# Kernel optimization log

Measured on AMD Instinct MI355X. Metric: run time of the kernel, lower is better.

The kernel has to match this reference:

```python
import jax, jax.numpy as jnp
import numpy as np

HID = 16  # comparator hidden channels, Conv1(2,16) -> Conv1(16,1)


def setup_inputs() -> dict:
    key = jax.random.key(0)
    k0, k1, k2 = jax.random.split(key, 3)
    B, N = 32, 512
    x = jax.random.normal(k0, (B, 1, N), dtype=jnp.float32)
    # xavier_uniform for 1x1 convs, zero bias (as in PermNet.__init__)
    g1 = (6.0 / (2 + HID)) ** 0.5
    g2 = (6.0 / (HID + 1)) ** 0.5
    w1 = jax.random.uniform(k1, (HID, 2), jnp.float32, -g1, g1)
    b1 = jnp.zeros((HID,), jnp.float32)
    w2 = jax.random.uniform(k2, (1, HID), jnp.float32, -g2, g2)
    b2 = jnp.zeros((1,), jnp.float32)
    lr = jnp.ones((1,), jnp.float32)  # learned step size, used via abs()
    return {"x": x, "w1": w1, "b1": b1, "w2": w2, "b2": b2, "lr": lr,
            "steps": 8, "temp": 1}


def reference(x, w1, b1, w2, b2, lr, steps, temp):
    B, C, N = x.shape  # C == 1 (scalar set elements)
    temp = jnp.asarray(temp, x.dtype)

    # --- Comparator: pairwise 1x1-conv MLP over all (i, j) pairs ---
    xi = jnp.broadcast_to(x[:, 0, :, None], (B, N, N))  # element i
    xj = jnp.broadcast_to(x[:, 0, None, :], (B, N, N))  # element j
    pairs = jnp.stack([xi, xj], axis=1)                  # (B, 2, N, N)
    h = jax.nn.relu(jnp.einsum('oc,bcij->boij', w1, pairs)
                    + b1[None, :, None, None])           # (B, HID, N, N)
    c = (jnp.einsum('oc,bcij->boij', w2, h)
         + b2[None, :, None, None])[:, 0]                # (B, N, N)
    c = c - jnp.swapaxes(c, -1, -2)  # antisymmetric ordering cost C(i,j)=-C(j,i)

    # --- calculate_assignment: iterative differentiable permutation ---
    # a[b, i, k] = weight of element i being placed at position k
    lr_abs = jnp.abs(lr)[0]
    a0 = jnp.full((B, N, N), 1.0 / N, dtype=x.dtype)

    def step(a, _):
        csum = jnp.cumsum(a, axis=-1)      # sum_{l<=k} a[., j, l]
        total = csum[..., -1:]
        left = csum - a                     # sum_{l<k}
        right = total - csum                # sum_{l>k}
        m = right - left                    # (B, N, N)
        # d(total cost)/d a_{ik} = sum_j C_{ij} * (right_{jk} - left_{jk})
        grad = jnp.einsum('bij,bjk->bik', c, m)
        a_new = jax.nn.softmax((a - lr_abs * grad) / temp, axis=-1)
        return a_new, None

    a, _ = jax.lax.scan(step, a0, None, length=steps)

    # --- apply_assignment: permute elements into positions ---
    y = jnp.einsum('bci,bik->bck', x, a)  # (B, 1, N)
    return y, a
```

## Files before the change

kernel.cpp:

```cpp
#include <hip/hip_runtime.h>
#include <hip/hip_bf16.h>
#include <math.h>

#define B_   32
#define N_   512
#define HID_ 16

typedef __attribute__((ext_vector_type(8))) short bf16x8;
typedef __attribute__((ext_vector_type(4))) float f32x4;

union U8 { ushort u[8]; uint4 v; };
union U4 { ushort u[4]; uint2 v; };

__device__ __forceinline__ ushort f2bf(float f) {
    __hip_bfloat16 h = __float2bfloat16(f);
    return *reinterpret_cast<ushort*>(&h);
}
__device__ __forceinline__ float bf2f(ushort u) {
    return __uint_as_float(((unsigned int)u) << 16);
}

__device__ __forceinline__ void gload16(const void* g, void* l) {
    __builtin_amdgcn_global_load_lds(
        (const __attribute__((address_space(1))) unsigned int*)g,
        (__attribute__((address_space(3))) unsigned int*)l,
        16, 0, 0);
}

__device__ __forceinline__ int pidx(int r, int c) {
    return r * N_ + ((c + ((r >> 3) << 2)) & (N_ - 1));
}

__global__ __launch_bounds__(256)
void init_kernel(const float* __restrict__ x,
                 const float* __restrict__ w1,
                 const float* __restrict__ b1,
                 const float* __restrict__ w2,
                 ushort* __restrict__ cB,
                 float* __restrict__ v)
{
    __shared__ float sw1[2*HID_], sb1[HID_], sw2[HID_];
    __shared__ float red[4];
    int tid = threadIdx.x;
    if (tid < 2*HID_) sw1[tid] = w1[tid];
    if (tid < HID_)   { sb1[tid] = b1[tid]; sw2[tid] = w2[tid]; }
    __syncthreads();

    int rowg = blockIdx.x * 2 + (tid >> 7);
    int b    = rowg >> 9;
    int col  = (tid & 127) * 4;
    float xi = x[rowg];
    float4 xj = *(const float4*)&x[b*N_ + col];
    float xjv[4] = {xj.x, xj.y, xj.z, xj.w};

    float s1[4] = {}, s2[4] = {};
#pragma unroll
    for (int o = 0; o < HID_; ++o) {
        float wa = sw1[2*o], wb = sw1[2*o+1], bo = sb1[o], wo = sw2[o];
        float Ao = fmaf(wa, xi, bo);
        float Co = fmaf(wb, xi, bo);
#pragma unroll
        for (int e = 0; e < 4; ++e) {
            s1[e] = fmaf(wo, fmaxf(fmaf(wb, xjv[e], Ao), 0.f), s1[e]);
            s2[e] = fmaf(wo, fmaxf(fmaf(wa, xjv[e], Co), 0.f), s2[e]);
        }
    }

    float rs = 0.f;
    U4 cb;
#pragma unroll
    for (int e = 0; e < 4; ++e) {
        float cv = s1[e] - s2[e];
        rs += cv;
        cb.u[e] = f2bf(cv);
    }
    *(uint2*)&cB[(size_t)rowg * N_ + col] = cb.v;

#pragma unroll
    for (int off = 1; off < 64; off <<= 1) rs += __shfl_xor(rs, off);
    int w = tid >> 6;
    if ((tid & 63) == 0) red[w] = rs;
    __syncthreads();
    if (tid < 2) v[blockIdx.x * 2 + tid] = red[2*tid] + red[2*tid + 1];
}

__global__ __launch_bounds__(512)
void fused_kernel(const ushort* __restrict__ cB,
                  const ushort* __restrict__ aTin,
                  const ushort* __restrict__ aBin,
                  ushort* __restrict__ aTout,
                  ushort* __restrict__ aBout,
                  float* __restrict__ aout,
                  const float* __restrict__ v,
                  const float* __restrict__ lr,
                  const int* __restrict__ temp,
                  int first, int last)
{
    __shared__ char smem[131072];
    float* Pl = (float*)smem;

    int iblk = blockIdx.x;
    int r8 = iblk & 7, m = iblk >> 3;
    int b  = r8 + ((m >> 3) << 3);
    int i0 = (m & 7) * 64;

    const size_t MATOFF = (size_t)b * N_ * N_;
    int tid = threadIdx.x, lane = tid & 63, w = tid >> 6;

    if (!first) {
        const ushort* Ag = cB   + MATOFF + (size_t)i0 * N_;
        const ushort* Bg = aTin + MATOFF + (size_t)(w * 64) * N_;
        char* Aw = smem + w * 16384;
        char* Bw = Aw + 8192;
        f32x4 acc[4][4] = {};

        for (int kt = 0; kt < N_/64; ++kt) {
            int j0 = kt * 64;
            asm volatile("s_waitcnt lgkmcnt(0)" ::: "memory");
#pragma unroll
            for (int g = 0; g < 8; ++g) {
                int r  = g*8 + (lane >> 3);
                int sl = lane & 7;
                int go = j0 + ((sl ^ (r & 7)) << 3);
                gload16(Ag + (size_t)r * N_ + go, Aw + g*1024 + lane*16);
                gload16(Bg + (size_t)r * N_ + go, Bw + g*1024 + lane*16);
            }
            asm volatile("s_waitcnt vmcnt(0)" ::: "memory");
            __builtin_amdgcn_sched_barrier(0);

#pragma unroll
            for (int kk = 0; kk < 2; ++kk) {
                bf16x8 af[4], bb[4];
#pragma unroll
                for (int f = 0; f < 4; ++f) {
                    int ra = f*16 + (lane & 15);
                    int sa = kk*4 + (lane >> 4);
                    af[f] = *(const bf16x8*)(Aw + ra*128 + ((sa ^ (ra & 7)) << 4));
                    bb[f] = *(const bf16x8*)(Bw + ra*128 + ((sa ^ (ra & 7)) << 4));
                }
#pragma unroll
                for (int i = 0; i < 4; ++i)
#pragma unroll
                    for (int j = 0; j < 4; ++j)
                        acc[i][j] = __builtin_amdgcn_mfma_f32_16x16x32_bf16(
                                        af[i], bb[j], acc[i][j], 0, 0, 0);
            }
        }
        __syncthreads();

        {
            int h = lane >> 4, cl = lane & 15;
#pragma unroll
            for (int i = 0; i < 4; ++i)
#pragma unroll
                for (int j = 0; j < 4; ++j)
#pragma unroll
                    for (int r = 0; r < 4; ++r)
                        Pl[pidx(i*16 + h*4 + r, w*64 + j*16 + cl)] = acc[i][j][r];
        }
        __syncthreads();
    }

    float lrv = fabsf(lr[0]);
    float ti  = 1.0f / (float)temp[0];

    for (int q = 0; q < 8; ++q) {
        int row  = w*8 + q;
        int grow = i0 + row;
        float vr = v[b*N_ + grow];

        float pv[8], av[8];
        if (first) {
#pragma unroll
            for (int e = 0; e < 8; ++e) { pv[e] = vr * (1.0f/N_); av[e] = 1.0f/N_; }
        } else {
            int rot = (row >> 3) << 2;
            int c0  = (lane*8     + rot) & (N_-1);
            int c1  = (lane*8 + 4 + rot) & (N_-1);
            f32x4 p0 = *(const f32x4*)&Pl[row*N_ + c0];
            f32x4 p1 = *(const f32x4*)&Pl[row*N_ + c1];
            pv[0]=p0[0]; pv[1]=p0[1]; pv[2]=p0[2]; pv[3]=p0[3];
            pv[4]=p1[0]; pv[5]=p1[1]; pv[6]=p1[2]; pv[7]=p1[3];
            U8 ab;
            ab.v = *(const uint4*)&aBin[MATOFF + (size_t)grow * N_ + lane*8];
#pragma unroll
            for (int e = 0; e < 8; ++e) av[e] = bf2f(ab.u[e]);
        }

        float cs[8], run = 0.f;
#pragma unroll
        for (int e = 0; e < 8; ++e) { run += pv[e]; cs[e] = run; }
        float laneTot = run;
        float sc = laneTot;
#pragma unroll
        for (int off = 1; off < 64; off <<= 1) {
            float t = __shfl_up(sc, off);
            if (lane >= off) sc += t;
        }
        float excl = sc - laneTot;

        float l[8];
#pragma unroll
        for (int e = 0; e < 8; ++e) {
            float Q    = excl + cs[e];
            float grad = vr - 2.f*Q + pv[e];
            l[e] = (av[e] - lrv*grad) * ti;
        }

        float mx = l[0];
#pragma unroll
        for (int e = 1; e < 8; ++e) mx = fmaxf(mx, l[e]);
#pragma unroll
        for (int off = 1; off < 64; off <<= 1) mx = fmaxf(mx, __shfl_xor(mx, off));

        float ex[8], s = 0.f;
#pragma unroll
        for (int e = 0; e < 8; ++e) { ex[e] = __expf(l[e] - mx); s += ex[e]; }
#pragma unroll
        for (int off = 1; off < 64; off <<= 1) s += __shfl_xor(s, off);

        float inv = 1.0f / s;
#pragma unroll
        for (int e = 0; e < 8; ++e) ex[e] *= inv;

        size_t gbase = MATOFF + (size_t)grow * N_ + lane*8;
        if (last) {
            *(float4*)&aout[gbase]     = make_float4(ex[0], ex[1], ex[2], ex[3]);
            *(float4*)&aout[gbase + 4] = make_float4(ex[4], ex[5], ex[6], ex[7]);
        } else {
            U8 ob;
#pragma unroll
            for (int e = 0; e < 8; ++e) ob.u[e] = f2bf(ex[e]);
            *(uint4*)&aBout[gbase] = ob.v;
            int rot = (row >> 3) << 2;
            int c0  = (lane*8     + rot) & (N_-1);
            int c1  = (lane*8 + 4 + rot) & (N_-1);
            *(f32x4*)&Pl[row*N_ + c0] = f32x4{ex[0], ex[1], ex[2], ex[3]};
            *(f32x4*)&Pl[row*N_ + c1] = f32x4{ex[4], ex[5], ex[6], ex[7]};
        }
    }

    if (!last) {
        __syncthreads();
#pragma unroll
        for (int p = 0; p < 8; ++p) {
            int k   = p*64 + (tid >> 3);
            int ii0 = (tid & 7) * 8;
            U8 ob;
#pragma unroll
            for (int e = 0; e < 8; ++e) ob.u[e] = f2bf(Pl[pidx(ii0 + e, k)]);
            *(uint4*)&aTout[MATOFF + (size_t)k * N_ + i0 + ii0] = ob.v;
        }
    }
}

__global__ __launch_bounds__(256)
void y_kernel(const float* __restrict__ x,
              const float* __restrict__ a,
              float* __restrict__ y)
{
    __shared__ float xs[N_];
    __shared__ float red[4][64];
    int b  = blockIdx.y;
    int k0 = blockIdx.x * 64;
    int tid = threadIdx.x;
    xs[tid]       = x[b*N_ + tid];
    xs[tid + 256] = x[b*N_ + tid + 256];
    __syncthreads();

    int kl = tid & 63, strip = tid >> 6;
    const float* A = a + (size_t)b * N_ * N_;
    float acc = 0.f;
    int i0 = strip * 128;
#pragma unroll 4
    for (int i = i0; i < i0 + 128; ++i)
        acc = fmaf(xs[i], A[(size_t)i * N_ + k0 + kl], acc);
    red[strip][kl] = acc;
    __syncthreads();
    if (strip == 0)
        y[b*N_ + k0 + kl] = red[0][kl] + red[1][kl] + red[2][kl] + red[3][kl];
}

extern "C" void kernel_launch(void* const* d_in, const int* in_sizes, int n_in,
                              void* d_out, int out_size, void* d_ws, size_t ws_size,
                              hipStream_t stream)
{
    const float* x  = (const float*)d_in[0];
    const float* w1 = (const float*)d_in[1];
    const float* b1 = (const float*)d_in[2];
    const float* w2 = (const float*)d_in[3];
    const float* lr   = (const float*)d_in[5];
    const int*   temp = (const int*)d_in[7];

    float* y = (float*)d_out;
    float* a = y + B_ * N_;

    const size_t MAT = (size_t)B_ * N_ * N_;
    ushort* cB  = (ushort*)d_ws;
    ushort* aT0 = cB  + MAT;
    ushort* aT1 = aT0 + MAT;
    ushort* aB0 = aT1 + MAT;
    ushort* aB1 = aB0 + MAT;
    float*  v   = (float*)(aB1 + MAT);

    hipLaunchKernelGGL(init_kernel, dim3(B_*N_/2), dim3(256), 0, stream,
                       x, w1, b1, w2, cB, v);

    hipLaunchKernelGGL(fused_kernel, dim3(256), dim3(512), 0, stream,
                       cB, aT1, aB1, aT0, aB0, a, v, lr, temp, 1, 0);
    int cur = 0;
    for (int s = 1; s < 7; ++s) {
        ushort* tin  = cur ? aT1 : aT0;
        ushort* binp = cur ? aB1 : aB0;
        ushort* tout = cur ? aT0 : aT1;
        ushort* bout = cur ? aB0 : aB1;
        hipLaunchKernelGGL(fused_kernel, dim3(256), dim3(512), 0, stream,
                           cB, tin, binp, tout, bout, a, v, lr, temp, 0, 0);
        cur ^= 1;
    }
    {
        ushort* tin  = cur ? aT1 : aT0;
        ushort* binp = cur ? aB1 : aB0;
        hipLaunchKernelGGL(fused_kernel, dim3(256), dim3(512), 0, stream,
                           cB, tin, binp, aT0, aB0, a, v, lr, temp, 0, 1);
    }
    hipLaunchKernelGGL(y_kernel, dim3(8, B_), dim3(256), 0, stream, x, a, y);
}
```

Measured before the change: 234.6 us.

## Fuse comparator into first step, keep A tile resident, fold y into last step

The separate comparator init kernel is removed: the first fused step now computes its cost rows and row sums directly, writes cB and v, and uses the sums from registers. In later steps the 64-row A block of the cost matrix is loaded into shared memory once per block, and only the B tiles are streamed per k-iteration, which halves the global traffic inside the loop. The final step accumulates x·a partial sums per block, and a small reduce kernel replaces the y kernel that re-read the full fp32 assignment. The trade-offs are more shared memory per block and a larger, more serial first step.

```diff
diff --git a/kernel.cpp b/kernel.cpp
--- a/kernel.cpp
+++ b/kernel.cpp
@@ -10,7 +10,6 @@
 typedef __attribute__((ext_vector_type(4))) float f32x4;
 
 union U8 { ushort u[8]; uint4 v; };
-union U4 { ushort u[4]; uint2 v; };
 
 __device__ __forceinline__ ushort f2bf(float f) {
     __hip_bfloat16 h = __float2bfloat16(f);
@@ -31,72 +30,25 @@
     return r * N_ + ((c + ((r >> 3) << 2)) & (N_ - 1));
 }
 
-__global__ __launch_bounds__(256)
-void init_kernel(const float* __restrict__ x,
-                 const float* __restrict__ w1,
-                 const float* __restrict__ b1,
-                 const float* __restrict__ w2,
-                 ushort* __restrict__ cB,
-                 float* __restrict__ v)
-{
-    __shared__ float sw1[2*HID_], sb1[HID_], sw2[HID_];
-    __shared__ float red[4];
-    int tid = threadIdx.x;
-    if (tid < 2*HID_) sw1[tid] = w1[tid];
-    if (tid < HID_)   { sb1[tid] = b1[tid]; sw2[tid] = w2[tid]; }
-    __syncthreads();
-
-    int rowg = blockIdx.x * 2 + (tid >> 7);
-    int b    = rowg >> 9;
-    int col  = (tid & 127) * 4;
-    float xi = x[rowg];
-    float4 xj = *(const float4*)&x[b*N_ + col];
-    float xjv[4] = {xj.x, xj.y, xj.z, xj.w};
-
-    float s1[4] = {}, s2[4] = {};
-#pragma unroll
-    for (int o = 0; o < HID_; ++o) {
-        float wa = sw1[2*o], wb = sw1[2*o+1], bo = sb1[o], wo = sw2[o];
-        float Ao = fmaf(wa, xi, bo);
-        float Co = fmaf(wb, xi, bo);
-#pragma unroll
-        for (int e = 0; e < 4; ++e) {
-            s1[e] = fmaf(wo, fmaxf(fmaf(wb, xjv[e], Ao), 0.f), s1[e]);
-            s2[e] = fmaf(wo, fmaxf(fmaf(wa, xjv[e], Co), 0.f), s2[e]);
-        }
-    }
-
-    float rs = 0.f;
-    U4 cb;
-#pragma unroll
-    for (int e = 0; e < 4; ++e) {
-        float cv = s1[e] - s2[e];
-        rs += cv;
-        cb.u[e] = f2bf(cv);
-    }
-    *(uint2*)&cB[(size_t)rowg * N_ + col] = cb.v;
-
-#pragma unroll
-    for (int off = 1; off < 64; off <<= 1) rs += __shfl_xor(rs, off);
-    int w = tid >> 6;
-    if ((tid & 63) == 0) red[w] = rs;
-    __syncthreads();
-    if (tid < 2) v[blockIdx.x * 2 + tid] = red[2*tid] + red[2*tid + 1];
-}
-
 __global__ __launch_bounds__(512)
-void fused_kernel(const ushort* __restrict__ cB,
+void fused_kernel(const float* __restrict__ x,
+                  const float* __restrict__ w1,
+                  const float* __restrict__ b1,
+                  const float* __restrict__ w2,
+                  ushort* __restrict__ cB,
                   const ushort* __restrict__ aTin,
                   const ushort* __restrict__ aBin,
                   ushort* __restrict__ aTout,
                   ushort* __restrict__ aBout,
                   float* __restrict__ aout,
-                  const float* __restrict__ v,
+                  float* __restrict__ vg,
+                  float* __restrict__ ypart,
                   const float* __restrict__ lr,
                   const int* __restrict__ temp,
                   int first, int last)
 {
     __shared__ char smem[131072];
+    __shared__ float sw1[2*HID_], sb1v[HID_], sw2v[HID_];
     float* Pl = (float*)smem;
 
     int iblk = blockIdx.x;
@@ -107,23 +59,71 @@
     const size_t MATOFF = (size_t)b * N_ * N_;
     int tid = threadIdx.x, lane = tid & 63, w = tid >> 6;
 
-    if (!first) {
+    float lrv = fabsf(lr[0]);
+    float ti  = 1.0f / (float)temp[0];
+    float vrq[8];
+
+    if (first) {
+        if (tid < 2*HID_) sw1[tid] = w1[tid];
+        if (tid < HID_)   { sb1v[tid] = b1[tid]; sw2v[tid] = w2[tid]; }
+        __syncthreads();
+        int k0 = lane * 8;
+        float4 xj0 = *(const float4*)&x[b*N_ + k0];
+        float4 xj1 = *(const float4*)&x[b*N_ + k0 + 4];
+        float xjv[8] = {xj0.x, xj0.y, xj0.z, xj0.w, xj1.x, xj1.y, xj1.z, xj1.w};
+        for (int q = 0; q < 8; ++q) {
+            int grow = i0 + w*8 + q;
+            float xi = x[b*N_ + grow];
+            float s1[8] = {}, s2[8] = {};
+            for (int o = 0; o < HID_; ++o) {
+                float wa = sw1[2*o], wb = sw1[2*o+1], bo = sb1v[o], wo = sw2v[o];
+                float Ao = fmaf(wa, xi, bo);
+                float Co = fmaf(wb, xi, bo);
+#pragma unroll
+                for (int e = 0; e < 8; ++e) {
+                    s1[e] = fmaf(wo, fmaxf(fmaf(wb, xjv[e], Ao), 0.f), s1[e]);
+                    s2[e] = fmaf(wo, fmaxf(fmaf(wa, xjv[e], Co), 0.f), s2[e]);
+                }
+            }
+            float rs = 0.f;
+            U8 cb;
+#pragma unroll
+            for (int e = 0; e < 8; ++e) {
+                float cv = s1[e] - s2[e];
+                rs += cv;
+                cb.u[e] = f2bf(cv);
+            }
+            *(uint4*)&cB[MATOFF + (size_t)grow * N_ + k0] = cb.v;
+#pragma unroll
+            for (int off = 1; off < 64; off <<= 1) rs += __shfl_xor(rs, off);
+            vrq[q] = rs;
+            if (lane == 0) vg[b*N_ + grow] = rs;
+        }
+    } else {
         const ushort* Ag = cB   + MATOFF + (size_t)i0 * N_;
         const ushort* Bg = aTin + MATOFF + (size_t)(w * 64) * N_;
-        char* Aw = smem + w * 16384;
-        char* Bw = Aw + 8192;
+        char* Asb = smem;
+        char* Bw  = smem + 65536 + w * 8192;
         f32x4 acc[4][4] = {};
 
-        for (int kt = 0; kt < N_/64; ++kt) {
-            int j0 = kt * 64;
+        {
+            int r = tid >> 3, sl = tid & 7;
+            const ushort* Asrc = Ag + (size_t)r * N_ + ((sl ^ (r & 7)) << 3);
+#pragma unroll
+            for (int c = 0; c < 8; ++c)
+                gload16(Asrc + c*64, Asb + c*8192 + tid*16);
+        }
+        asm volatile("s_waitcnt vmcnt(0)" ::: "memory");
+        __syncthreads();
+
+        for (int kt = 0; kt < 8; ++kt) {
             asm volatile("s_waitcnt lgkmcnt(0)" ::: "memory");
 #pragma unroll
             for (int g = 0; g < 8; ++g) {
                 int r  = g*8 + (lane >> 3);
                 int sl = lane & 7;
-                int go = j0 + ((sl ^ (r & 7)) << 3);
-                gload16(Ag + (size_t)r * N_ + go, Aw + g*1024 + lane*16);
-                gload16(Bg + (size_t)r * N_ + go, Bw + g*1024 + lane*16);
+                gload16(Bg + (size_t)r * N_ + kt*64 + ((sl ^ (r & 7)) << 3),
+                        Bw + g*1024 + lane*16);
             }
             asm volatile("s_waitcnt vmcnt(0)" ::: "memory");
             __builtin_amdgcn_sched_barrier(0);
@@ -135,7 +135,7 @@
                 for (int f = 0; f < 4; ++f) {
                     int ra = f*16 + (lane & 15);
                     int sa = kk*4 + (lane >> 4);
-                    af[f] = *(const bf16x8*)(Aw + ra*128 + ((sa ^ (ra & 7)) << 4));
+                    af[f] = *(const bf16x8*)(Asb + kt*8192 + ra*128 + ((sa ^ (ra & 7)) << 4));
                     bb[f] = *(const bf16x8*)(Bw + ra*128 + ((sa ^ (ra & 7)) << 4));
                 }
 #pragma unroll
@@ -161,13 +161,12 @@
         __syncthreads();
     }
 
-    float lrv = fabsf(lr[0]);
-    float ti  = 1.0f / (float)temp[0];
+    float ysum[8] = {};
 
     for (int q = 0; q < 8; ++q) {
         int row  = w*8 + q;
         int grow = i0 + row;
-        float vr = v[b*N_ + grow];
+        float vr = first ? vrq[q] : vg[b*N_ + grow];
 
         float pv[8], av[8];
         if (first) {
@@ -227,6 +226,9 @@
         if (last) {
             *(float4*)&aout[gbase]     = make_float4(ex[0], ex[1], ex[2], ex[3]);
             *(float4*)&aout[gbase + 4] = make_float4(ex[4], ex[5], ex[6], ex[7]);
+            float xr = x[b*N_ + grow];
+#pragma unroll
+            for (int e = 0; e < 8; ++e) ysum[e] = fmaf(xr, ex[e], ysum[e]);
         } else {
             U8 ob;
 #pragma unroll
@@ -251,34 +253,28 @@
             for (int e = 0; e < 8; ++e) ob.u[e] = f2bf(Pl[pidx(ii0 + e, k)]);
             *(uint4*)&aTout[MATOFF + (size_t)k * N_ + i0 + ii0] = ob.v;
         }
-    }
-}
-
-__global__ __launch_bounds__(256)
-void y_kernel(const float* __restrict__ x,
-              const float* __restrict__ a,
-              float* __restrict__ y)
+    } else {
+        __syncthreads();
+        float* yred = (float*)smem;
+        *(f32x4*)&yred[w*512 + lane*8]     = f32x4{ysum[0], ysum[1], ysum[2], ysum[3]};
+        *(f32x4*)&yred[w*512 + lane*8 + 4] = f32x4{ysum[4], ysum[5], ysum[6], ysum[7]};
+        __syncthreads();
+        float acc2 = 0.f;
+#pragma unroll
+        for (int wv = 0; wv < 8; ++wv) acc2 += yred[wv*512 + tid];
+        ypart[(size_t)(b*8 + (i0 >> 6)) * 512 + tid] = acc2;
+    }
+}
+
+__global__ __launch_bounds__(512)
+void y_reduce_kernel(const float* __restrict__ ypart, float* __restrict__ y)
 {
-    __shared__ float xs[N_];
-    __shared__ float red[4][64];
-    int b  = blockIdx.y;
-    int k0 = blockIdx.x * 64;
-    int tid = threadIdx.x;
-    xs[tid]       = x[b*N_ + tid];
-    xs[tid + 256] = x[b*N_ + tid + 256];
-    __syncthreads();
-
-    int kl = tid & 63, strip = tid >> 6;
-    const float* A = a + (size_t)b * N_ * N_;
+    int b = blockIdx.x, k = threadIdx.x;
     float acc = 0.f;
-    int i0 = strip * 128;
-#pragma unroll 4
-    for (int i = i0; i < i0 + 128; ++i)
-        acc = fmaf(xs[i], A[(size_t)i * N_ + k0 + kl], acc);
-    red[strip][kl] = acc;
-    __syncthreads();
-    if (strip == 0)
-        y[b*N_ + k0 + kl] = red[0][kl] + red[1][kl] + red[2][kl] + red[3][kl];
+#pragma unroll
+    for (int t = 0; t < 8; ++t)
+        acc += ypart[(size_t)(b*8 + t) * 512 + k];
+    y[b*N_ + k] = acc;
 }
 
 extern "C" void kernel_launch(void* const* d_in, const int* in_sizes, int n_in,
@@ -296,18 +292,17 @@
     float* a = y + B_ * N_;
 
     const size_t MAT = (size_t)B_ * N_ * N_;
-    ushort* cB  = (ushort*)d_ws;
-    ushort* aT0 = cB  + MAT;
-    ushort* aT1 = aT0 + MAT;
-    ushort* aB0 = aT1 + MAT;
-    ushort* aB1 = aB0 + MAT;
-    float*  v   = (float*)(aB1 + MAT);
-
-    hipLaunchKernelGGL(init_kernel, dim3(B_*N_/2), dim3(256), 0, stream,
-                       x, w1, b1, w2, cB, v);
+    ushort* cB    = (ushort*)d_ws;
+    ushort* aT0   = cB  + MAT;
+    ushort* aT1   = aT0 + MAT;
+    ushort* aB0   = aT1 + MAT;
+    ushort* aB1   = aB0 + MAT;
+    float*  v     = (float*)(aB1 + MAT);
+    float*  ypart = v + B_ * N_;
 
     hipLaunchKernelGGL(fused_kernel, dim3(256), dim3(512), 0, stream,
-                       cB, aT1, aB1, aT0, aB0, a, v, lr, temp, 1, 0);
+                       x, w1, b1, w2, cB, aT1, aB1, aT0, aB0, a, v, ypart,
+                       lr, temp, 1, 0);
     int cur = 0;
     for (int s = 1; s < 7; ++s) {
         ushort* tin  = cur ? aT1 : aT0;
@@ -315,14 +310,16 @@
         ushort* tout = cur ? aT0 : aT1;
         ushort* bout = cur ? aB0 : aB1;
         hipLaunchKernelGGL(fused_kernel, dim3(256), dim3(512), 0, stream,
-                           cB, tin, binp, tout, bout, a, v, lr, temp, 0, 0);
+                           x, w1, b1, w2, cB, tin, binp, tout, bout, a, v, ypart,
+                           lr, temp, 0, 0);
         cur ^= 1;
     }
     {
         ushort* tin  = cur ? aT1 : aT0;
         ushort* binp = cur ? aB1 : aB0;
         hipLaunchKernelGGL(fused_kernel, dim3(256), dim3(512), 0, stream,
-                           cB, tin, binp, aT0, aB0, a, v, lr, temp, 0, 1);
-    }
-    hipLaunchKernelGGL(y_kernel, dim3(8, B_), dim3(256), 0, stream, x, a, y);
-}
+                           x, w1, b1, w2, cB, tin, binp, aT0, aB0, a, v, ypart,
+                           lr, temp, 0, 1);
+    }
+    hipLaunchKernelGGL(y_reduce_kernel, dim3(B_), dim3(512), 0, stream, ypart, y);
+}
```

Measured after the change: 223.8 us. 1.05x faster.
